# Kernel optimization log

Measured on AMD Instinct MI355X. Metric: run time of the kernel, lower is better.

## Reference

```python
import jax, jax.numpy as jnp
import numpy as np

EPS_IN = 1e-5  # torch InstanceNorm2d default eps

def _gather(a, idx):
    # a: [B,C,N], idx: [B,M,K] -> [B,C,M,K]
    return jax.vmap(lambda ab, ib: ab[:, ib])(a, idx)

def _inorm(v, w, b):
    # InstanceNorm2d over spatial dims (M,K), per batch per channel, affine
    mean = v.mean(axis=(2, 3), keepdims=True)
    var = v.var(axis=(2, 3), keepdims=True)
    return (v - mean) * jax.lax.rsqrt(var + EPS_IN) * w[None, :, None, None] + b[None, :, None, None]

def setup_inputs() -> dict:
    key = jax.random.key(0)
    ks = jax.random.split(key, 10)
    B, N, M, K = 4, 8192, 8192, 16
    Cin, Cout, KS, DIM = 64, 64, 16, 3
    inp = {
        'x': jax.random.normal(ks[0], (B, Cin, N), dtype=jnp.float32),
        'pos': jax.random.normal(ks[1], (B, DIM, N), dtype=jnp.float32),
        'support_points': jax.random.normal(ks[2], (B, DIM, M), dtype=jnp.float32),
        'neighbors_indices': jax.random.randint(ks[3], (B, M, K), 0, N, dtype=jnp.int32),
        'alpha': jnp.ones((1,), jnp.float32),
        'beta': jnp.ones((1,), jnp.float32),
        'norm_radius': jnp.ones((1,), jnp.float32),
        'fc1_w': jax.random.normal(ks[4], (KS, DIM), jnp.float32) * 0.3,
        'fc2_w': jax.random.normal(ks[5], (KS, 2 * KS), jnp.float32) * 0.15,
        'fc3_w': jax.random.normal(ks[6], (KS, 2 * KS), jnp.float32) * 0.15,
        'bn1_w': jnp.ones((KS,), jnp.float32), 'bn1_b': jnp.zeros((KS,), jnp.float32),
        'bn2_w': jnp.ones((KS,), jnp.float32), 'bn2_b': jnp.zeros((KS,), jnp.float32),
        'cv_w': jax.random.normal(ks[7], (Cout, Cin, KS), jnp.float32) * (1.0 / np.sqrt(Cin * KS)),
    }
    return inp

def reference(x, pos, support_points, neighbors_indices, alpha, beta, norm_radius,
              fc1_w, fc2_w, fc3_w, bn1_w, bn1_b, bn2_w, bn2_b, cv_w):
    # eval mode, adaptive_normalization=True, K>1 branch (K=16)
    pos_g = _gather(pos, neighbors_indices)            # [B,3,M,K]
    x_g = _gather(x, neighbors_indices)                # [B,Cin,M,K]
    pts = pos_g - support_points[:, :, :, None]        # [B,3,M,K]
    K = pts.shape[3]

    # distances computed on detached pts in torch
    d = jnp.sqrt((jax.lax.stop_gradient(pts) ** 2).sum(axis=1))  # [B,M,K]
    pts = pts / norm_radius
    dw = jax.nn.sigmoid(-alpha * d + beta)             # [B,M,K]
    dws = dw.sum(axis=2, keepdims=True)
    dws = dws + (dws == 0).astype(dw.dtype) + 1e-6
    dw = (dw / dws * K)[:, None]                       # [B,1,M,K]

    mat = jax.nn.relu(_inorm(jnp.einsum('oc,bcmk->bomk', fc1_w, pts), bn1_w, bn1_b))  # [B,16,M,K]
    mp1 = jnp.max(mat * dw, axis=3, keepdims=True)
    mat = jnp.concatenate([mat, jnp.broadcast_to(mp1, mat.shape)], axis=1)            # [B,32,M,K]
    mat = jax.nn.relu(_inorm(jnp.einsum('oc,bcmk->bomk', fc2_w, mat), bn2_w, bn2_b))
    mp2 = jnp.max(mat * dw, axis=3, keepdims=True)
    mat = jnp.concatenate([mat, jnp.broadcast_to(mp2, mat.shape)], axis=1)
    mat = jax.nn.relu(jnp.einsum('oc,bcmk->bomk', fc3_w, mat)) * dw                   # [B,16,M,K]

    # features = x_g^T @ mat over K, then 1x16 conv contracting the 16-kernel axis
    feat = jnp.einsum('bcmk,bjmk->bcmj', x_g, mat)     # [B,Cin,M,16]
    out = jnp.einsum('ocj,bcmj->bom', cv_w, feat)      # [B,Cout,M]
    return out
```

## Files before the change

### kernel.cpp

```cpp
#include <hip/hip_runtime.h>
#include <math.h>

#define BB 4
#define NN 8192
#define MM 8192
#define KK 16

#define WS_CVB_BYTE  2048
#define WS_XT_BYTE   (WS_CVB_BYTE + 131072)
#define WS_PT_BYTE   (WS_XT_BYTE + 4194304)
#define WS_MOMP_BYTE (WS_PT_BYTE + 524288)
#define WS_P2_BYTE   (WS_MOMP_BYTE + 6144)

#define OV_STRIDE 1048
#define M3_STRIDE 400

typedef __bf16 bhalf;
typedef bhalf bhalf8 __attribute__((ext_vector_type(8)));
typedef float f32x4 __attribute__((ext_vector_type(4)));
typedef ushort ushort8v __attribute__((ext_vector_type(8)));
typedef ushort ushort4v __attribute__((ext_vector_type(4)));

static __device__ __forceinline__ ushort f2b(float f) {
    return __builtin_bit_cast(ushort, (__bf16)f);
}

__device__ __forceinline__ float gsum16(float v) {
#pragma unroll
    for (int mask = 8; mask >= 1; mask >>= 1) v += __shfl_xor(v, mask);
    return v;
}
__device__ __forceinline__ float gmax16(float v) {
#pragma unroll
    for (int mask = 8; mask >= 1; mask >>= 1) v = fmaxf(v, __shfl_xor(v, mask));
    return v;
}

__global__ __launch_bounds__(256) void k_pre(const float* __restrict__ x,
                                             const float* __restrict__ pos,
                                             const float* __restrict__ sup,
                                             const int* __restrict__ nbr,
                                             const float* __restrict__ cv,
                                             float* __restrict__ momp,
                                             ushort* __restrict__ cvb,
                                             ushort* __restrict__ xT,
                                             float* __restrict__ posT) {
    int bid = blockIdx.x, t = threadIdx.x;
    if (bid < 512) {
        int b = bid >> 7, n0 = (bid & 127) * 64;
        __shared__ ushort tile[64 * 66];
        const float* xb = x + (size_t)b * 64 * NN;
#pragma unroll
        for (int i = 0; i < 16; i++) {
            int c = i * 4 + (t >> 6), n = t & 63;
            tile[c * 66 + n] = f2b(xb[(size_t)c * NN + n0 + n]);
        }
        __syncthreads();
#pragma unroll
        for (int i = 0; i < 16; i++) {
            int n = i * 4 + (t >> 6), c = t & 63;
            xT[((size_t)b * NN + n0 + n) * 64 + c] = tile[c * 66 + n];
        }
        int nl = t >> 2, d = t & 3;
        float v = (d < 3) ? pos[((size_t)b * 3 + d) * NN + n0 + nl] : 0.f;
        posT[((size_t)b * NN + n0 + nl) * 4 + d] = v;
    } else if (bid < 576) {
        int e = (bid - 512) * 1024 + t * 4;
        float4 cvv = *(const float4*)(cv + e);
        ushort4v o = {f2b(cvv.x), f2b(cvv.y), f2b(cvv.z), f2b(cvv.w)};
        *(ushort4v*)(cvb + e) = o;
    } else {
        __shared__ float redm[36];
        int rem = bid - 576;
        int b = rem & 3, m = (rem >> 2) * 256 + t;
        const float* posb = pos + (size_t)b * 3 * NN;
        float sx = sup[((size_t)b * 3 + 0) * MM + m];
        float sy = sup[((size_t)b * 3 + 1) * MM + m];
        float sz = sup[((size_t)b * 3 + 2) * MM + m];
        const int* nb = nbr + ((size_t)b * MM + m) * KK;
        float s[9] = {0, 0, 0, 0, 0, 0, 0, 0, 0};
#pragma unroll
        for (int k = 0; k < KK; k++) {
            int id = nb[k];
            float px = posb[id] - sx, py = posb[NN + id] - sy, pz = posb[2 * NN + id] - sz;
            s[0] += px; s[1] += py; s[2] += pz;
            s[3] += px * px; s[4] += py * py; s[5] += pz * pz;
            s[6] += px * py; s[7] += px * pz; s[8] += py * pz;
        }
#pragma unroll
        for (int i = 0; i < 9; i++) {
            float v = s[i];
#pragma unroll
            for (int off = 32; off >= 1; off >>= 1) v += __shfl_down(v, off);
            if ((t & 63) == 0) redm[(t >> 6) * 9 + i] = v;
        }
        __syncthreads();
        if (t < 9) momp[rem * 12 + t] = redm[t] + redm[9 + t] + redm[18 + t] + redm[27 + t];
    }
}

__global__ __launch_bounds__(256) void k_stats2(const float* __restrict__ sup,
                                                const int* __restrict__ nbr,
                                                const float* __restrict__ alpha_,
                                                const float* __restrict__ beta_,
                                                const float* __restrict__ nr_,
                                                const float* __restrict__ fc1,
                                                const float* __restrict__ fc2,
                                                const float* __restrict__ bn1w,
                                                const float* __restrict__ bn1b,
                                                const float* __restrict__ posT,
                                                const float* __restrict__ momp,
                                                float* __restrict__ p2) {
    __shared__ float sc1[16], bi1[16], momr[9], red[4 * 33];
    int t = threadIdx.x, b = blockIdx.y;
    if (t < 9) {
        float s = 0.f;
#pragma unroll
        for (int g = 0; g < 32; g++) s += momp[(4 * g + b) * 12 + t];
        momr[t] = s;
    }
    __syncthreads();
    if (t < 16) {
        float inv = 1.f / (float)(MM * KK);
        float inr = 1.f / nr_[0];
        float mux = momr[0] * inv * inr, muy = momr[1] * inv * inr, muz = momr[2] * inv * inr;
        float i2 = inv * inr * inr;
        float w0 = fc1[t * 3], w1v = fc1[t * 3 + 1], w2v = fc1[t * 3 + 2];
        float mean = w0 * mux + w1v * muy + w2v * muz;
        float ey2 = w0 * w0 * momr[3] * i2 + w1v * w1v * momr[4] * i2 + w2v * w2v * momr[5] * i2 +
                    2.f * (w0 * w1v * momr[6] * i2 + w0 * w2v * momr[7] * i2 + w1v * w2v * momr[8] * i2);
        float var = fmaxf(ey2 - mean * mean, 0.f);
        float rs = rsqrtf(var + 1e-5f);
        sc1[t] = bn1w[t] * rs;
        bi1[t] = bn1b[t] - mean * sc1[t];
    }
    __syncthreads();
    int mi = t >> 2, kq = t & 3;
    int m = blockIdx.x * 64 + mi;
    float alpha = alpha_[0], beta = beta_[0], inr = 1.f / nr_[0];
    float sx = sup[((size_t)b * 3 + 0) * MM + m];
    float sy = sup[((size_t)b * 3 + 1) * MM + m];
    float sz = sup[((size_t)b * 3 + 2) * MM + m];
    const int* nb = nbr + ((size_t)b * MM + m) * KK + kq * 4;

    float q1m[16], G1[16], G2[16];
#pragma unroll
    for (int j = 0; j < 16; j++) { q1m[j] = 0.f; G1[j] = 0.f; G2[j] = 0.f; }
    float S = 0.f;
#pragma unroll
    for (int kk = 0; kk < 4; kk++) {
        int id = nb[kk];
        float4 pv = *(const float4*)(posT + ((size_t)b * NN + id) * 4);
        float rx = pv.x - sx, ry = pv.y - sy, rz = pv.z - sz;
        float dd = sqrtf(rx * rx + ry * ry + rz * rz);
        float srk = 1.f / (1.f + expf(alpha * dd - beta));
        S += srk;
        float nxv = rx * inr, nyv = ry * inr, nzv = rz * inr;
        float m1c[16];
#pragma unroll
        for (int j = 0; j < 16; j++) {
            float y = fc1[j * 3] * nxv + fc1[j * 3 + 1] * nyv + fc1[j * 3 + 2] * nzv;
            m1c[j] = fmaxf(y * sc1[j] + bi1[j], 0.f);
            q1m[j] = fmaxf(q1m[j], m1c[j] * srk);
        }
#pragma unroll
        for (int c = 0; c < 16; c++) {
            float g = 0.f;
#pragma unroll
            for (int q = 0; q < 4; q++) {
                float4 v = *(const float4*)(fc2 + c * 32 + q * 4);
                g += v.x * m1c[q * 4] + v.y * m1c[q * 4 + 1] +
                     v.z * m1c[q * 4 + 2] + v.w * m1c[q * 4 + 3];
            }
            G1[c] += g; G2[c] += g * g;
        }
    }
    S += __shfl_xor(S, 1); S += __shfl_xor(S, 2);
#pragma unroll
    for (int j = 0; j < 16; j++) {
        q1m[j] = fmaxf(q1m[j], __shfl_xor(q1m[j], 1));
        q1m[j] = fmaxf(q1m[j], __shfl_xor(q1m[j], 2));
    }
    S = S + (S == 0.f ? 1.f : 0.f) + 1e-6f;
    float fac = 16.f / S;
#pragma unroll
    for (int c = 0; c < 16; c++) {
        float h2 = 0.f;
#pragma unroll
        for (int q = 0; q < 4; q++) {
            float4 v = *(const float4*)(fc2 + c * 32 + 16 + q * 4);
            h2 += v.x * q1m[q * 4] + v.y * q1m[q * 4 + 1] +
                  v.z * q1m[q * 4 + 2] + v.w * q1m[q * 4 + 3];
        }
        h2 *= fac;
        float s2p = G1[c] + 4.f * h2;
        float q2p = G2[c] + 2.f * h2 * G1[c] + 4.f * h2 * h2;
#pragma unroll
        for (int off = 32; off >= 1; off >>= 1) {
            s2p += __shfl_down(s2p, off);
            q2p += __shfl_down(q2p, off);
        }
        if ((t & 63) == 0) {
            red[(t >> 6) * 33 + c] = s2p;
            red[(t >> 6) * 33 + 16 + c] = q2p;
        }
    }
    __syncthreads();
    if (t < 32)
        p2[((size_t)b * 128 + blockIdx.x) * 32 + t] =
            red[t] + red[33 + t] + red[66 + t] + red[99 + t];
}

__global__ __launch_bounds__(256) void k_final(const float* __restrict__ sup,
                                               const int* __restrict__ nbr,
                                               const float* __restrict__ alpha_,
                                               const float* __restrict__ beta_,
                                               const float* __restrict__ nr_,
                                               const float* __restrict__ fc1,
                                               const float* __restrict__ fc2,
                                               const float* __restrict__ fc3,
                                               const float* __restrict__ bn1w,
                                               const float* __restrict__ bn1b,
                                               const float* __restrict__ bn2w,
                                               const float* __restrict__ bn2b,
                                               const float* __restrict__ momp,
                                               const float* __restrict__ p2,
                                               const ushort* __restrict__ cvb,
                                               const ushort* __restrict__ xT,
                                               const float* __restrict__ posT,
                                               float* __restrict__ out) {
    __shared__ float s1[16], b1[16], s2[16], b2[16];
    __shared__ float momr[9], p2r[8 * 33];
    __shared__ __align__(16) ushort ov[16 * OV_STRIDE];
    __shared__ __align__(16) ushort m3l[16 * M3_STRIDE];

    int t = threadIdx.x;
    int b = blockIdx.y;
    int m0 = blockIdx.x * 16;
    int w = t >> 6, l = t & 63;
    int lk = l & 15, kg = l >> 4;
    int ps = t >> 4, ks = t & 15;

    int idxt = nbr[((size_t)b * MM + m0 + ps) * KK + ks];
    float4 pf = *(const float4*)(posT + ((size_t)b * NN + idxt) * 4);
    const ushort8v* xrow = (const ushort8v*)(xT + ((size_t)b * NN + idxt) * 64);
    ushort8v g0 = xrow[0], g1 = xrow[1], g2 = xrow[2], g3 = xrow[3];
    ushort8v g4 = xrow[4], g5 = xrow[5], g6 = xrow[6], g7 = xrow[7];
    float4 w2b0 = *(const float4*)(fc2 + ks * 32 + 16);
    float4 w2b1 = *(const float4*)(fc2 + ks * 32 + 20);
    float4 w2b2 = *(const float4*)(fc2 + ks * 32 + 24);
    float4 w2b3 = *(const float4*)(fc2 + ks * 32 + 28);
    float4 w3b0 = *(const float4*)(fc3 + ks * 32 + 16);
    float4 w3b1 = *(const float4*)(fc3 + ks * 32 + 20);
    float4 w3b2 = *(const float4*)(fc3 + ks * 32 + 24);
    float4 w3b3 = *(const float4*)(fc3 + ks * 32 + 28);

    float alpha = alpha_[0], beta = beta_[0], inr = 1.f / nr_[0];

    if (t < 9) {
        float s = 0.f;
#pragma unroll
        for (int g = 0; g < 32; g++) s += momp[(4 * g + b) * 12 + t];
        momr[t] = s;
    }
    {
        int c = t & 31, ch = t >> 5;
        float s = 0.f;
#pragma unroll
        for (int g = 0; g < 16; g++) s += p2[((size_t)b * 128 + ch * 16 + g) * 32 + c];
        p2r[ch * 33 + c] = s;
    }
    __syncthreads();
    if (t < 16) {
        float inv = 1.f / (float)(MM * KK);
        float mux = momr[0] * inv * inr, muy = momr[1] * inv * inr, muz = momr[2] * inv * inr;
        float i2 = inv * inr * inr;
        float w0 = fc1[t * 3], wa = fc1[t * 3 + 1], wb = fc1[t * 3 + 2];
        float mean = w0 * mux + wa * muy + wb * muz;
        float ey2 = w0 * w0 * momr[3] * i2 + wa * wa * momr[4] * i2 + wb * wb * momr[5] * i2 +
                    2.f * (w0 * wa * momr[6] * i2 + w0 * wb * momr[7] * i2 + wa * wb * momr[8] * i2);
        float var = fmaxf(ey2 - mean * mean, 0.f);
        float rs = rsqrtf(var + 1e-5f);
        s1[t] = bn1w[t] * rs;
        b1[t] = bn1b[t] - mean * s1[t];
        float sum2 = 0.f, ssq2 = 0.f;
#pragma unroll
        for (int ch = 0; ch < 8; ch++) {
            sum2 += p2r[ch * 33 + t];
            ssq2 += p2r[ch * 33 + 16 + t];
        }
        float mean2 = sum2 * inv;
        float var2 = fmaxf(ssq2 * inv - mean2 * mean2, 0.f);
        float rs2 = rsqrtf(var2 + 1e-5f);
        s2[t] = bn2w[t] * rs2;
        b2[t] = bn2b[t] - mean2 * s2[t];
    }
    __syncthreads();

    {
        int mm = m0 + ps;
        float rx = pf.x - sup[((size_t)b * 3 + 0) * MM + mm];
        float ry = pf.y - sup[((size_t)b * 3 + 1) * MM + mm];
        float rz = pf.z - sup[((size_t)b * 3 + 2) * MM + mm];
        float dd = sqrtf(rx * rx + ry * ry + rz * rz);
        float sr = 1.f / (1.f + expf(alpha * dd - beta));
        float S = gsum16(sr);
        S = S + (S == 0.f ? 1.f : 0.f) + 1e-6f;
        float dwk = sr * (16.f / S);
        float nxv = rx * inr, nyv = ry * inr, nzv = rz * inr;

        float m1v[16], mp1[16];
#pragma unroll
        for (int j = 0; j < 16; j++) {
            float y = fc1[j * 3] * nxv + fc1[j * 3 + 1] * nyv + fc1[j * 3 + 2] * nzv;
            m1v[j] = fmaxf(y * s1[j] + b1[j], 0.f);
        }
#pragma unroll
        for (int j = 0; j < 16; j++) mp1[j] = gmax16(m1v[j] * dwk);

        float h2own = w2b0.x * mp1[0] + w2b0.y * mp1[1] + w2b0.z * mp1[2] + w2b0.w * mp1[3]
                    + w2b1.x * mp1[4] + w2b1.y * mp1[5] + w2b1.z * mp1[6] + w2b1.w * mp1[7]
                    + w2b2.x * mp1[8] + w2b2.y * mp1[9] + w2b2.z * mp1[10] + w2b2.w * mp1[11]
                    + w2b3.x * mp1[12] + w2b3.y * mp1[13] + w2b3.z * mp1[14] + w2b3.w * mp1[15];
        int pbase = l & 48;
        float m2v[16], mp2[16];
#pragma unroll
        for (int c = 0; c < 16; c++) {
            float a = 0.f;
#pragma unroll
            for (int q = 0; q < 4; q++) {
                float4 v = *(const float4*)(fc2 + c * 32 + q * 4);
                a += v.x * m1v[q * 4] + v.y * m1v[q * 4 + 1] + v.z * m1v[q * 4 + 2] + v.w * m1v[q * 4 + 3];
            }
            a += __shfl(h2own, pbase + c);
            m2v[c] = fmaxf(a * s2[c] + b2[c], 0.f);
        }
#pragma unroll
        for (int c = 0; c < 16; c++) mp2[c] = gmax16(m2v[c] * dwk);

        float h3own = w3b0.x * mp2[0] + w3b0.y * mp2[1] + w3b0.z * mp2[2] + w3b0.w * mp2[3]
                    + w3b1.x * mp2[4] + w3b1.y * mp2[5] + w3b1.z * mp2[6] + w3b1.w * mp2[7]
                    + w3b2.x * mp2[8] + w3b2.y * mp2[9] + w3b2.z * mp2[10] + w3b2.w * mp2[11]
                    + w3b3.x * mp2[12] + w3b3.y * mp2[13] + w3b3.z * mp2[14] + w3b3.w * mp2[15];
        ushort* m3p = m3l + ps * M3_STRIDE;
#pragma unroll
        for (int j = 0; j < 16; j++) {
            float a = 0.f;
#pragma unroll
            for (int q = 0; q < 4; q++) {
                float4 v = *(const float4*)(fc3 + j * 32 + q * 4);
                a += v.x * m2v[q * 4] + v.y * m2v[q * 4 + 1] + v.z * m2v[q * 4 + 2] + v.w * m2v[q * 4 + 3];
            }
            a += __shfl(h3own, pbase + j);
            m3p[j * 24 + ks] = f2b(fmaxf(a, 0.f) * dwk);
        }
    }

    {
        ushort* ovp = ov + ps * OV_STRIDE;
#define STG(gv, h) _Pragma("unroll") for (int i2 = 0; i2 < 8; i2++) ovp[((h) * 8 + i2) * 16 + ks] = (ushort)gv[i2];
        STG(g0, 0) STG(g1, 1) STG(g2, 2) STG(g3, 3)
        STG(g4, 4) STG(g5, 5) STG(g6, 6) STG(g7, 7)
#undef STG
    }
    __syncthreads();

    const f32x4 zz = {0.f, 0.f, 0.f, 0.f};

#pragma unroll
    for (int pp = 0; pp < 4; pp++) {
        int p = w * 4 + pp;
        bhalf8 afr = {};
        if (kg < 2) afr = __builtin_bit_cast(bhalf8, *(ushort8v*)(m3l + p * M3_STRIDE + lk * 24 + kg * 8));
        ushort* ovb = ov + p * OV_STRIDE;
#pragma unroll
        for (int cb = 0; cb < 4; cb++) {
            bhalf8 bfr = {};
            if (kg < 2) bfr = __builtin_bit_cast(bhalf8, *(ushort8v*)(ovb + (cb * 16 + lk) * 16 + kg * 8));
            f32x4 dF = __builtin_amdgcn_mfma_f32_16x16x32_bf16(afr, bfr, zz, 0, 0, 0);
            ushort4v fw = {f2b(dF[0]), f2b(dF[1]), f2b(dF[2]), f2b(dF[3])};
            *(ushort4v*)(ovb + (cb * 16 + lk) * 16 + kg * 4) = fw;
        }
    }
    __syncthreads();

    {
        const ushort* arow = cvb + (size_t)(w * 16 + lk) * 1024;
        const ushort* brow = ov + lk * OV_STRIDE;
        f32x4 acc = zz;
#pragma unroll
        for (int kt = 0; kt < 32; kt++) {
            bhalf8 au = __builtin_bit_cast(bhalf8, *(const ushort8v*)(arow + kt * 32 + kg * 8));
            bhalf8 bu = __builtin_bit_cast(bhalf8, *(const ushort8v*)(brow + kt * 32 + kg * 8));
            acc = __builtin_amdgcn_mfma_f32_16x16x32_bf16(au, bu, acc, 0, 0, 0);
        }
#pragma unroll
        for (int r = 0; r < 4; r++) {
            int o = w * 16 + kg * 4 + r;
            out[((size_t)(b * 64 + o)) * MM + m0 + lk] = acc[r];
        }
    }
}

extern "C" void kernel_launch(void* const* d_in, const int* in_sizes, int n_in,
                              void* d_out, int out_size, void* d_ws, size_t ws_size,
                              hipStream_t stream) {
    const float* x    = (const float*)d_in[0];
    const float* pos  = (const float*)d_in[1];
    const float* sup  = (const float*)d_in[2];
    const int*   nbr  = (const int*)d_in[3];
    const float* alp  = (const float*)d_in[4];
    const float* bet  = (const float*)d_in[5];
    const float* nr   = (const float*)d_in[6];
    const float* fc1  = (const float*)d_in[7];
    const float* fc2  = (const float*)d_in[8];
    const float* fc3  = (const float*)d_in[9];
    const float* bn1w = (const float*)d_in[10];
    const float* bn1b = (const float*)d_in[11];
    const float* bn2w = (const float*)d_in[12];
    const float* bn2b = (const float*)d_in[13];
    const float* cv   = (const float*)d_in[14];
    float* out = (float*)d_out;
    ushort* cvb  = (ushort*)((char*)d_ws + WS_CVB_BYTE);
    ushort* xT   = (ushort*)((char*)d_ws + WS_XT_BYTE);
    float*  posT = (float*)((char*)d_ws + WS_PT_BYTE);
    float*  momp = (float*)((char*)d_ws + WS_MOMP_BYTE);
    float*  p2   = (float*)((char*)d_ws + WS_P2_BYTE);

    k_pre<<<704, 256, 0, stream>>>(x, pos, sup, nbr, cv, momp, cvb, xT, posT);
    k_stats2<<<dim3(128, BB), 256, 0, stream>>>(sup, nbr, alp, bet, nr, fc1, fc2,
                                                bn1w, bn1b, posT, momp, p2);
    k_final<<<dim3(512, BB), 256, 0, stream>>>(sup, nbr, alp, bet, nr, fc1, fc2, fc3,
                                               bn1w, bn1b, bn2w, bn2b, momp, p2,
                                               cvb, xT, posT, out);
}
```

Measured before the change: 108.5 us.

## Hoist norm-stat finalization into tiny kernel, use DPP reductions, split MFMA accumulators

Adds a small k_fin kernel that reduces the partial moments once per batch and writes the scale/bias vectors, so each of the 2048 k_final blocks loads only 64 floats instead of re-reducing the partial sums. The 16-lane sum/max reductions switch from shuffles to DPP row rotates, the final conv MFMA chain is split across two accumulators to break the dependency, and the LDS strides are changed. The extra kernel launch adds a serialization point and launch latency, and the new LDS strides may change bank-conflict behavior.

```diff
diff --git a/kernel.cpp b/kernel.cpp
--- a/kernel.cpp
+++ b/kernel.cpp
@@ -11,9 +11,10 @@
 #define WS_PT_BYTE   (WS_XT_BYTE + 4194304)
 #define WS_MOMP_BYTE (WS_PT_BYTE + 524288)
 #define WS_P2_BYTE   (WS_MOMP_BYTE + 6144)
-
-#define OV_STRIDE 1048
-#define M3_STRIDE 400
+#define WS_SB_BYTE   (WS_P2_BYTE + 65536)
+
+#define OV_STRIDE 1040
+#define M3_STRIDE 384
 
 typedef __bf16 bhalf;
 typedef bhalf bhalf8 __attribute__((ext_vector_type(8)));
@@ -25,14 +26,23 @@
     return __builtin_bit_cast(ushort, (__bf16)f);
 }
 
+template <int CTRL>
+__device__ __forceinline__ float dpp_rot(float v) {
+    int r = __builtin_amdgcn_update_dpp(0, __builtin_bit_cast(int, v), CTRL, 0xF, 0xF, true);
+    return __builtin_bit_cast(float, r);
+}
+__device__ __forceinline__ float gmax16(float v) {
+    v = fmaxf(v, dpp_rot<0x121>(v));
+    v = fmaxf(v, dpp_rot<0x122>(v));
+    v = fmaxf(v, dpp_rot<0x124>(v));
+    v = fmaxf(v, dpp_rot<0x128>(v));
+    return v;
+}
 __device__ __forceinline__ float gsum16(float v) {
-#pragma unroll
-    for (int mask = 8; mask >= 1; mask >>= 1) v += __shfl_xor(v, mask);
-    return v;
-}
-__device__ __forceinline__ float gmax16(float v) {
-#pragma unroll
-    for (int mask = 8; mask >= 1; mask >>= 1) v = fmaxf(v, __shfl_xor(v, mask));
+    v += dpp_rot<0x121>(v);
+    v += dpp_rot<0x122>(v);
+    v += dpp_rot<0x124>(v);
+    v += dpp_rot<0x128>(v);
     return v;
 }
 
@@ -211,6 +221,60 @@
             red[t] + red[33 + t] + red[66 + t] + red[99 + t];
 }
 
+__global__ __launch_bounds__(256) void k_fin(const float* __restrict__ momp,
+                                             const float* __restrict__ p2,
+                                             const float* __restrict__ fc1,
+                                             const float* __restrict__ bn1w,
+                                             const float* __restrict__ bn1b,
+                                             const float* __restrict__ bn2w,
+                                             const float* __restrict__ bn2b,
+                                             const float* __restrict__ nr_,
+                                             float* __restrict__ sb) {
+    __shared__ float red[8 * 33], momr[9];
+    int b = blockIdx.x, t = threadIdx.x;
+    int c = t & 31, ch = t >> 5;
+    float s = 0.f;
+#pragma unroll
+    for (int g = 0; g < 16; g++) s += p2[((size_t)b * 128 + ch * 16 + g) * 32 + c];
+    red[ch * 33 + c] = s;
+    if (t < 9) {
+        float v = 0.f;
+#pragma unroll
+        for (int g = 0; g < 32; g++) v += momp[(4 * g + b) * 12 + t];
+        momr[t] = v;
+    }
+    __syncthreads();
+    if (t < 16) {
+        float inv = 1.f / (float)(MM * KK);
+        float inr = 1.f / nr_[0];
+        float mux = momr[0] * inv * inr, muy = momr[1] * inv * inr, muz = momr[2] * inv * inr;
+        float i2 = inv * inr * inr;
+        float w0 = fc1[t * 3], wa = fc1[t * 3 + 1], wb = fc1[t * 3 + 2];
+        float mean = w0 * mux + wa * muy + wb * muz;
+        float ey2 = w0 * w0 * momr[3] * i2 + wa * wa * momr[4] * i2 + wb * wb * momr[5] * i2 +
+                    2.f * (w0 * wa * momr[6] * i2 + w0 * wb * momr[7] * i2 + wa * wb * momr[8] * i2);
+        float var = fmaxf(ey2 - mean * mean, 0.f);
+        float rs = rsqrtf(var + 1e-5f);
+        float s1v = bn1w[t] * rs;
+        float b1v = bn1b[t] - mean * s1v;
+        float sum2 = 0.f, ssq2 = 0.f;
+#pragma unroll
+        for (int chh = 0; chh < 8; chh++) {
+            sum2 += red[chh * 33 + t];
+            ssq2 += red[chh * 33 + 16 + t];
+        }
+        float mean2 = sum2 * inv;
+        float var2 = fmaxf(ssq2 * inv - mean2 * mean2, 0.f);
+        float rs2 = rsqrtf(var2 + 1e-5f);
+        float s2v = bn2w[t] * rs2;
+        float b2v = bn2b[t] - mean2 * s2v;
+        sb[b * 64 + t] = s1v;
+        sb[b * 64 + 16 + t] = b1v;
+        sb[b * 64 + 32 + t] = s2v;
+        sb[b * 64 + 48 + t] = b2v;
+    }
+}
+
 __global__ __launch_bounds__(256) void k_final(const float* __restrict__ sup,
                                                const int* __restrict__ nbr,
                                                const float* __restrict__ alpha_,
@@ -219,18 +283,12 @@
                                                const float* __restrict__ fc1,
                                                const float* __restrict__ fc2,
                                                const float* __restrict__ fc3,
-                                               const float* __restrict__ bn1w,
-                                               const float* __restrict__ bn1b,
-                                               const float* __restrict__ bn2w,
-                                               const float* __restrict__ bn2b,
-                                               const float* __restrict__ momp,
-                                               const float* __restrict__ p2,
+                                               const float* __restrict__ sb,
                                                const ushort* __restrict__ cvb,
                                                const ushort* __restrict__ xT,
                                                const float* __restrict__ posT,
                                                float* __restrict__ out) {
-    __shared__ float s1[16], b1[16], s2[16], b2[16];
-    __shared__ float momr[9], p2r[8 * 33];
+    __shared__ float sbl[64];
     __shared__ __align__(16) ushort ov[16 * OV_STRIDE];
     __shared__ __align__(16) ushort m3l[16 * M3_STRIDE];
 
@@ -257,44 +315,7 @@
 
     float alpha = alpha_[0], beta = beta_[0], inr = 1.f / nr_[0];
 
-    if (t < 9) {
-        float s = 0.f;
-#pragma unroll
-        for (int g = 0; g < 32; g++) s += momp[(4 * g + b) * 12 + t];
-        momr[t] = s;
-    }
-    {
-        int c = t & 31, ch = t >> 5;
-        float s = 0.f;
-#pragma unroll
-        for (int g = 0; g < 16; g++) s += p2[((size_t)b * 128 + ch * 16 + g) * 32 + c];
-        p2r[ch * 33 + c] = s;
-    }
-    __syncthreads();
-    if (t < 16) {
-        float inv = 1.f / (float)(MM * KK);
-        float mux = momr[0] * inv * inr, muy = momr[1] * inv * inr, muz = momr[2] * inv * inr;
-        float i2 = inv * inr * inr;
-        float w0 = fc1[t * 3], wa = fc1[t * 3 + 1], wb = fc1[t * 3 + 2];
-        float mean = w0 * mux + wa * muy + wb * muz;
-        float ey2 = w0 * w0 * momr[3] * i2 + wa * wa * momr[4] * i2 + wb * wb * momr[5] * i2 +
-                    2.f * (w0 * wa * momr[6] * i2 + w0 * wb * momr[7] * i2 + wa * wb * momr[8] * i2);
-        float var = fmaxf(ey2 - mean * mean, 0.f);
-        float rs = rsqrtf(var + 1e-5f);
-        s1[t] = bn1w[t] * rs;
-        b1[t] = bn1b[t] - mean * s1[t];
-        float sum2 = 0.f, ssq2 = 0.f;
-#pragma unroll
-        for (int ch = 0; ch < 8; ch++) {
-            sum2 += p2r[ch * 33 + t];
-            ssq2 += p2r[ch * 33 + 16 + t];
-        }
-        float mean2 = sum2 * inv;
-        float var2 = fmaxf(ssq2 * inv - mean2 * mean2, 0.f);
-        float rs2 = rsqrtf(var2 + 1e-5f);
-        s2[t] = bn2w[t] * rs2;
-        b2[t] = bn2b[t] - mean2 * s2[t];
-    }
+    if (t < 64) sbl[t] = sb[b * 64 + t];
     __syncthreads();
 
     {
@@ -313,7 +334,7 @@
 #pragma unroll
         for (int j = 0; j < 16; j++) {
             float y = fc1[j * 3] * nxv + fc1[j * 3 + 1] * nyv + fc1[j * 3 + 2] * nzv;
-            m1v[j] = fmaxf(y * s1[j] + b1[j], 0.f);
+            m1v[j] = fmaxf(y * sbl[j] + sbl[16 + j], 0.f);
         }
 #pragma unroll
         for (int j = 0; j < 16; j++) mp1[j] = gmax16(m1v[j] * dwk);
@@ -333,7 +354,7 @@
                 a += v.x * m1v[q * 4] + v.y * m1v[q * 4 + 1] + v.z * m1v[q * 4 + 2] + v.w * m1v[q * 4 + 3];
             }
             a += __shfl(h2own, pbase + c);
-            m2v[c] = fmaxf(a * s2[c] + b2[c], 0.f);
+            m2v[c] = fmaxf(a * sbl[32 + c] + sbl[48 + c], 0.f);
         }
 #pragma unroll
         for (int c = 0; c < 16; c++) mp2[c] = gmax16(m2v[c] * dwk);
@@ -387,17 +408,20 @@
     {
         const ushort* arow = cvb + (size_t)(w * 16 + lk) * 1024;
         const ushort* brow = ov + lk * OV_STRIDE;
-        f32x4 acc = zz;
-#pragma unroll
-        for (int kt = 0; kt < 32; kt++) {
-            bhalf8 au = __builtin_bit_cast(bhalf8, *(const ushort8v*)(arow + kt * 32 + kg * 8));
-            bhalf8 bu = __builtin_bit_cast(bhalf8, *(const ushort8v*)(brow + kt * 32 + kg * 8));
-            acc = __builtin_amdgcn_mfma_f32_16x16x32_bf16(au, bu, acc, 0, 0, 0);
+        f32x4 acc0 = zz, acc1 = zz;
+#pragma unroll
+        for (int kt = 0; kt < 32; kt += 2) {
+            bhalf8 au0 = __builtin_bit_cast(bhalf8, *(const ushort8v*)(arow + kt * 32 + kg * 8));
+            bhalf8 bu0 = __builtin_bit_cast(bhalf8, *(const ushort8v*)(brow + kt * 32 + kg * 8));
+            bhalf8 au1 = __builtin_bit_cast(bhalf8, *(const ushort8v*)(arow + (kt + 1) * 32 + kg * 8));
+            bhalf8 bu1 = __builtin_bit_cast(bhalf8, *(const ushort8v*)(brow + (kt + 1) * 32 + kg * 8));
+            acc0 = __builtin_amdgcn_mfma_f32_16x16x32_bf16(au0, bu0, acc0, 0, 0, 0);
+            acc1 = __builtin_amdgcn_mfma_f32_16x16x32_bf16(au1, bu1, acc1, 0, 0, 0);
         }
 #pragma unroll
         for (int r = 0; r < 4; r++) {
             int o = w * 16 + kg * 4 + r;
-            out[((size_t)(b * 64 + o)) * MM + m0 + lk] = acc[r];
+            out[((size_t)(b * 64 + o)) * MM + m0 + lk] = acc0[r] + acc1[r];
         }
     }
 }
@@ -426,11 +450,12 @@
     float*  posT = (float*)((char*)d_ws + WS_PT_BYTE);
     float*  momp = (float*)((char*)d_ws + WS_MOMP_BYTE);
     float*  p2   = (float*)((char*)d_ws + WS_P2_BYTE);
+    float*  sb   = (float*)((char*)d_ws + WS_SB_BYTE);
 
     k_pre<<<704, 256, 0, stream>>>(x, pos, sup, nbr, cv, momp, cvb, xT, posT);
     k_stats2<<<dim3(128, BB), 256, 0, stream>>>(sup, nbr, alp, bet, nr, fc1, fc2,
                                                 bn1w, bn1b, posT, momp, p2);
+    k_fin<<<BB, 256, 0, stream>>>(momp, p2, fc1, bn1w, bn1b, bn2w, bn2b, nr, sb);
     k_final<<<dim3(512, BB), 256, 0, stream>>>(sup, nbr, alp, bet, nr, fc1, fc2, fc3,
-                                               bn1w, bn1b, bn2w, bn2b, momp, p2,
-                                               cvb, xT, posT, out);
-}
+                                               sb, cvb, xT, posT, out);
+}
```

New measurement: 96.89 us. 10.7% less time.
